# Performance work log

Measured on AMD Instinct MI355X. Metric: run time of the kernel, lower is better.

## Reference

```python
import jax, jax.numpy as jnp
import numpy as np

N = 4096      # batch size
D = 512       # flattened feature dim
C = 128       # num classes / output dim
K = 2         # knn k (module default)
ALPHA = 0.0005


def _safe_sqrt(d2):
    # sqrt with zero (not nan) gradient at exactly 0, matching torch.norm
    d2 = jnp.maximum(d2, 0.0)
    safe = jnp.where(d2 > 0, d2, 1.0)
    return jnp.where(d2 > 0, jnp.sqrt(safe), 0.0)


def _pairwise_dist(a):
    # a: [n, d] -> [n, n] euclidean distances via gram trick
    sq = jnp.sum(a * a, axis=1)
    d2 = sq[:, None] + sq[None, :] - 2.0 * (a @ a.T)
    return _safe_sqrt(d2)


def setup_inputs() -> dict:
    key = jax.random.key(0)
    k1, k2, k3, k4 = jax.random.split(key, 4)
    x_batch = jax.random.normal(k1, (N, D), jnp.float32)
    y_batch = jax.random.randint(k2, (N,), 0, C)
    y_output = jax.random.normal(k3, (N, C), jnp.float32)
    W = jax.random.normal(k4, (D, C), jnp.float32) * 0.02
    b = jnp.zeros((C,), jnp.float32)
    return {"x_batch": x_batch, "y_batch": y_batch, "y_output": y_output, "W": W, "b": b}


def reference(x_batch, y_batch, y_output, W, b):
    n = x_batch.shape[0]
    # ---- loss_function(net(x_batch), y_batch): linear net + cross entropy ----
    logits = x_batch.reshape(n, -1) @ W + b                     # [n, C]
    logp = jax.nn.log_softmax(logits, axis=-1)
    loss = -jnp.mean(jnp.take_along_axis(logp, y_batch[:, None], axis=1))

    # ---- compute_weights_based_on_knn (vectorized) ----
    dx = _pairwise_dist(x_batch.reshape(n, -1))                 # [n, n]
    order = jnp.argsort(dx, axis=1)                             # sklearn kneighbors order
    d_sorted = jnp.take_along_axis(dx, order, axis=1)           # sorted distances (sklearn d)
    e_d = jnp.exp(-d_sorted)                                    # [n, n]
    nbr = order[:, :K + 1]                                      # [n, K+1] raw indices
    rows = jnp.arange(n)[:, None]
    nbr_mask = jnp.zeros((n, n), jnp.float32).at[rows, nbr].set(1.0)  # j in neighbors[i]
    same = (y_batch[:, None] == y_batch[None, :]).astype(jnp.float32)
    # w_diff = w_int - 0; w_int[i,j] = e_d[i,j] (raw-j index into sorted e_d, as in source)
    w_diff = e_d * nbr_mask * same                              # [n, n]

    # ---- weighted_output: sum_ij ||y_out[i]-y_out[j]|| * w_diff[i,j] ----
    dy = _pairwise_dist(y_output)                               # [n, n]
    reg = jnp.sum(dy * w_diff)

    return loss + ALPHA * reg
```

## Files before the change

### kernel.cpp

```cpp
#include <hip/hip_runtime.h>
#include <math.h>
#include <stdint.h>

#define N 4096
#define D 512
#define C 128
#define ALPHA 0.0005f
#define NT_TILES 32
#define TRI (NT_TILES * (NT_TILES + 1) / 2)
#define NTILE (TRI + N / 128)
#define GRID_FUSED 1024

typedef __bf16 bf16x8 __attribute__((ext_vector_type(8)));
typedef float f32x4 __attribute__((ext_vector_type(4)));

__device__ __forceinline__ void wg_barrier_lgkm() {
    asm volatile("s_waitcnt lgkmcnt(0)\n\ts_barrier" ::: "memory");
}

__global__ __launch_bounds__(256) void prep_kernel(const float* __restrict__ x,
                                                   float* __restrict__ sq,
                                                   float* __restrict__ dot0,
                                                   __bf16* __restrict__ xb,
                                                   const float* __restrict__ W,
                                                   __bf16* __restrict__ Wtb,
                                                   unsigned* __restrict__ cnt,
                                                   unsigned* __restrict__ qhead) {
    if (blockIdx.x >= N / 4) {
        const int tid = (blockIdx.x - N / 4) * 256 + threadIdx.x;
        const int k = tid >> 7;
        const int n = tid & 127;
        Wtb[(size_t)n * D + k] = (__bf16)W[tid];
        if (blockIdx.x == N / 4 && threadIdx.x == 0) *qhead = 0u;
        return;
    }
    const int i = blockIdx.x * 4 + (threadIdx.x >> 6);
    const int l = threadIdx.x & 63;
    const float* xp = x + (size_t)i * D + l * 8;
    const float4 v0 = *(const float4*)(xp);
    const float4 v1 = *(const float4*)(xp + 4);
    const float4 u0 = *(const float4*)(x + l * 8);
    const float4 u1 = *(const float4*)(x + l * 8 + 4);
    float s1 = v0.x * v0.x + v0.y * v0.y + v0.z * v0.z + v0.w * v0.w
             + v1.x * v1.x + v1.y * v1.y + v1.z * v1.z + v1.w * v1.w;
    float s2 = v0.x * u0.x + v0.y * u0.y + v0.z * u0.z + v0.w * u0.w
             + v1.x * u1.x + v1.y * u1.y + v1.z * u1.z + v1.w * u1.w;
    bf16x8 o;
    o[0] = (__bf16)v0.x; o[1] = (__bf16)v0.y; o[2] = (__bf16)v0.z; o[3] = (__bf16)v0.w;
    o[4] = (__bf16)v1.x; o[5] = (__bf16)v1.y; o[6] = (__bf16)v1.z; o[7] = (__bf16)v1.w;
    *(bf16x8*)(xb + (size_t)i * D + l * 8) = o;
    for (int off = 32; off; off >>= 1) {
        s1 += __shfl_down(s1, off);
        s2 += __shfl_down(s2, off);
    }
    if (l == 0) { sq[i] = s1; dot0[i] = s2; cnt[i] = 0u; }
}

__global__ __launch_bounds__(256) void fused_mfma(const __bf16* __restrict__ xb,
                                                  const __bf16* __restrict__ Wtb,
                                                  const float* __restrict__ sq,
                                                  const float* __restrict__ dot0,
                                                  const int* __restrict__ y,
                                                  const float* __restrict__ b,
                                                  unsigned* __restrict__ cnt,
                                                  float* __restrict__ lossrow,
                                                  unsigned* __restrict__ qhead) {
    __shared__ __bf16 Alds[2][128 * 32];
    __shared__ __bf16 Blds[2][128 * 32];
    __shared__ float rmax[128][2];
    __shared__ float rsum[128][2];
    __shared__ int bidS;
    const int t = threadIdx.x;
    const int w = t >> 6, l = t & 63;
    const int wy = w >> 1, wx = w & 1;
    const int kg = l >> 4, lr = l & 15;

    const int e0 = t, e1 = t + 256;
    const int r0 = e0 >> 2, c0 = e0 & 3;
    const int r1 = e1 >> 2, c1 = e1 & 3;
    const int sc0 = (c0 ^ (r0 & 3) ^ ((r0 >> 2) & 3)) & 3;
    const int sc1 = (c1 ^ (r1 & 3) ^ ((r1 >> 2) & 3)) & 3;

    for (;;) {
        if (t == 0) bidS = (int)atomicAdd(qhead, 1u);
        __syncthreads();
        const int bid = bidS;
        if (bid >= NTILE) break;

        const bool isCE = (bid >= TRI);
        int bi, bj;
        bool diag = false;
        const __bf16* Bbase;
        if (isCE) {
            bi = (bid - TRI) * 128;
            bj = 0;
            Bbase = Wtb;
        } else {
            int tj = (int)((sqrtf(8.f * (float)bid + 1.f) - 1.f) * 0.5f);
            while (tj * (tj + 1) / 2 > bid) --tj;
            while ((tj + 1) * (tj + 2) / 2 <= bid) ++tj;
            const int ti = bid - tj * (tj + 1) / 2;
            bi = ti * 128;
            bj = tj * 128;
            diag = (ti == tj);
            Bbase = xb + (size_t)bj * D;
        }
        const __bf16* Abase = xb + (size_t)bi * D;

        f32x4 acc[4][4];
        const f32x4 zero = {0.f, 0.f, 0.f, 0.f};
#pragma unroll
        for (int mt = 0; mt < 4; ++mt)
#pragma unroll
            for (int nt = 0; nt < 4; ++nt) acc[mt][nt] = zero;

        const __bf16* Ap0 = Abase + (size_t)r0 * D + sc0 * 8;
        const __bf16* Ap1 = Abase + (size_t)r1 * D + sc1 * 8;
        const __bf16* Bp0 = Bbase + (size_t)r0 * D + sc0 * 8;
        const __bf16* Bp1 = Bbase + (size_t)r1 * D + sc1 * 8;

        uint4 ra0 = *(const uint4*)Ap0;
        uint4 ra1 = *(const uint4*)Ap1;
        uint4 rb0, rb1;
        if (!diag) { rb0 = *(const uint4*)Bp0; rb1 = *(const uint4*)Bp1; }

        for (int k = 0; k < 16; ++k) {
            const int buf = k & 1;
            *(uint4*)((char*)Alds[buf] + e0 * 16) = ra0;
            *(uint4*)((char*)Alds[buf] + e1 * 16) = ra1;
            if (!diag) {
                *(uint4*)((char*)Blds[buf] + e0 * 16) = rb0;
                *(uint4*)((char*)Blds[buf] + e1 * 16) = rb1;
            }
            if (k < 15) {
                const int off = (k + 1) * 32;
                ra0 = *(const uint4*)(Ap0 + off);
                ra1 = *(const uint4*)(Ap1 + off);
                if (!diag) {
                    rb0 = *(const uint4*)(Bp0 + off);
                    rb1 = *(const uint4*)(Bp1 + off);
                }
            }
            wg_barrier_lgkm();
            const __bf16* Al = Alds[buf];
            const __bf16* Bl = diag ? Alds[buf] : Blds[buf];
            bf16x8 av[4], bv[4];
#pragma unroll
            for (int mt = 0; mt < 4; ++mt) {
                const int row = wy * 64 + mt * 16 + lr;
                const int slot = (kg ^ (row & 3) ^ ((row >> 2) & 3)) & 3;
                av[mt] = *(const bf16x8*)(Al + row * 32 + slot * 8);
            }
#pragma unroll
            for (int nt = 0; nt < 4; ++nt) {
                const int row = wx * 64 + nt * 16 + lr;
                const int slot = (kg ^ (row & 3) ^ ((row >> 2) & 3)) & 3;
                bv[nt] = *(const bf16x8*)(Bl + row * 32 + slot * 8);
            }
#pragma unroll
            for (int mt = 0; mt < 4; ++mt)
#pragma unroll
                for (int nt = 0; nt < 4; ++nt)
                    acc[mt][nt] = __builtin_amdgcn_mfma_f32_16x16x32_bf16(av[mt], bv[nt], acc[mt][nt], 0, 0, 0);
        }

        if (isCE) {
            int jn[4]; float bb[4];
#pragma unroll
            for (int nt = 0; nt < 4; ++nt) { jn[nt] = wx * 64 + nt * 16 + lr; bb[nt] = b[jn[nt]]; }
#pragma unroll
            for (int mt = 0; mt < 4; ++mt)
#pragma unroll
                for (int r = 0; r < 4; ++r) {
                    float m = acc[mt][0][r] + bb[0];
#pragma unroll
                    for (int nt = 1; nt < 4; ++nt) m = fmaxf(m, acc[mt][nt][r] + bb[nt]);
                    m = fmaxf(m, __shfl_xor(m, 1));
                    m = fmaxf(m, __shfl_xor(m, 2));
                    m = fmaxf(m, __shfl_xor(m, 4));
                    m = fmaxf(m, __shfl_xor(m, 8));
                    if (lr == 0) rmax[wy * 64 + mt * 16 + kg * 4 + r][wx] = m;
                }
            __syncthreads();
            float mrow[4][4];
#pragma unroll
            for (int mt = 0; mt < 4; ++mt)
#pragma unroll
                for (int r = 0; r < 4; ++r) {
                    const int ri = wy * 64 + mt * 16 + kg * 4 + r;
                    mrow[mt][r] = fmaxf(rmax[ri][0], rmax[ri][1]);
                    float s = 0.f;
#pragma unroll
                    for (int nt = 0; nt < 4; ++nt) s += expf(acc[mt][nt][r] + bb[nt] - mrow[mt][r]);
                    s += __shfl_xor(s, 1);
                    s += __shfl_xor(s, 2);
                    s += __shfl_xor(s, 4);
                    s += __shfl_xor(s, 8);
                    if (lr == 0) rsum[ri][wx] = s;
                }
            __syncthreads();
#pragma unroll
            for (int mt = 0; mt < 4; ++mt)
#pragma unroll
                for (int r = 0; r < 4; ++r) {
                    const int ri = wy * 64 + mt * 16 + kg * 4 + r;
                    const int i = bi + ri;
                    const float s = rsum[ri][0] + rsum[ri][1];
                    const int yi = y[i];
#pragma unroll
                    for (int nt = 0; nt < 4; ++nt)
                        if (jn[nt] == yi)
                            lossrow[i] = -(acc[mt][nt][r] + bb[nt] - mrow[mt][r] - logf(s));
                }
        } else {
            const float sq0 = sq[0];
            int jn[4]; float sqj[4], thrj[4];
#pragma unroll
            for (int nt = 0; nt < 4; ++nt) {
                jn[nt] = bj + wx * 64 + nt * 16 + lr;
                sqj[nt] = sq[jn[nt]];
                thrj[nt] = sq0 - 2.0f * dot0[jn[nt]];
            }
            unsigned cj[4] = {0u, 0u, 0u, 0u};
#pragma unroll
            for (int mt = 0; mt < 4; ++mt)
#pragma unroll
                for (int r = 0; r < 4; ++r) {
                    const int i = bi + wy * 64 + mt * 16 + kg * 4 + r;
                    const float thri = sq0 - 2.0f * dot0[i];
                    const float sqi = sq[i];
                    unsigned ci = 0;
                    if (diag) {
#pragma unroll
                        for (int nt = 0; nt < 4; ++nt) {
                            const float d = acc[mt][nt][r];
                            const int j = jn[nt];
                            if (sqj[nt] - 2.0f * d < thri && j != i && j != 0) ++ci;
                        }
                    } else {
#pragma unroll
                        for (int nt = 0; nt < 4; ++nt) {
                            const float d = acc[mt][nt][r];
                            if (sqj[nt] - 2.0f * d < thri) ++ci;
                            if (sqi - 2.0f * d < thrj[nt] && i != 0) ++cj[nt];
                        }
                    }
                    ci += __shfl_xor((int)ci, 1);
                    ci += __shfl_xor((int)ci, 2);
                    ci += __shfl_xor((int)ci, 4);
                    ci += __shfl_xor((int)ci, 8);
                    if (lr == 0 && ci) atomicAdd(&cnt[i], ci);
                }
            if (!diag) {
#pragma unroll
                for (int nt = 0; nt < 4; ++nt) {
                    unsigned v = cj[nt];
                    v += __shfl_xor((int)v, 16);
                    v += __shfl_xor((int)v, 32);
                    if (l < 16 && v) atomicAdd(&cnt[jn[nt]], v);
                }
            }
        }
    }
}

__global__ __launch_bounds__(1024) void final_kernel(const float* __restrict__ lossrow,
                                                     const unsigned* __restrict__ cnt,
                                                     const int* __restrict__ y,
                                                     const float* __restrict__ Y,
                                                     float* __restrict__ out) {
    const int t = threadIdx.x;
    const int y0 = y[0];
    double ls = 0.0, rs = 0.0;
    for (int i = t; i < N; i += 1024) {
        ls += (double)lossrow[i];
        if (i > 0 && y[i] == y0 && cnt[i] <= 1u) {
            float d2 = 0.f;
            for (int c = 0; c < C; ++c) {
                float d = Y[(size_t)i * C + c] - Y[c];
                d2 += d * d;
            }
            rs += (double)sqrtf(fmaxf(d2, 0.f));
        }
    }
    for (int o = 32; o; o >>= 1) {
        ls += __shfl_down(ls, o);
        rs += __shfl_down(rs, o);
    }
    __shared__ double dl[16], dr[16];
    if ((t & 63) == 0) { dl[t >> 6] = ls; dr[t >> 6] = rs; }
    __syncthreads();
    if (t == 0) {
        double L = 0.0, R = 0.0;
        for (int k = 0; k < 16; ++k) { L += dl[k]; R += dr[k]; }
        out[0] = (float)(L / (double)N + (double)ALPHA * R);
    }
}

extern "C" void kernel_launch(void* const* d_in, const int* in_sizes, int n_in,
                              void* d_out, int out_size, void* d_ws, size_t ws_size,
                              hipStream_t stream) {
    const float* x  = (const float*)d_in[0];
    const int*   y  = (const int*)d_in[1];
    const float* Y  = (const float*)d_in[2];
    const float* W  = (const float*)d_in[3];
    const float* b  = (const float*)d_in[4];
    float* out = (float*)d_out;

    float* wsf      = (float*)d_ws;
    float* lossrow  = wsf;
    float* sq       = wsf + N;
    float* dot0     = wsf + 2 * N;
    unsigned* cnt   = (unsigned*)(wsf + 3 * N);
    __bf16* xb      = (__bf16*)(wsf + 4 * N);
    __bf16* Wtb     = (__bf16*)((char*)xb + (size_t)N * D * 2);
    unsigned* qhead = (unsigned*)((char*)Wtb + (size_t)C * D * 2);

    prep_kernel<<<N / 4 + 256, 256, 0, stream>>>(x, sq, dot0, xb, W, Wtb, cnt, qhead);
    fused_mfma<<<GRID_FUSED, 256, 0, stream>>>(xb, Wtb, sq, dot0, y, b, cnt, lossrow, qhead);
    final_kernel<<<1, 1024, 0, stream>>>(lossrow, cnt, y, Y, out);
}
```

Measured before the change: 119.1 us.

## Replace persistent tile queue with static 64x128 tiles, async LDS loads, parallel final reduction

The persistent atomic work-queue over 128x128 triangular tiles is replaced by a static grid of 64x128 strip tiles, one block per tile, plus 64-row cross-entropy tiles. Tiles are loaded with global_load_lds async copies into a single LDS buffer, with two barriers per k-step in place of the register-prefetch double buffer. The single-block final kernel becomes a 32-block reduction that combines its partial sums through double atomics and a completion counter. The smaller tiles and more blocks aim to improve load balance and occupancy, at the cost of lower data reuse per tile and less overlap between loads and MFMA work.

New measurement: 107.7 us. 9.6% less time.

```diff
diff --git a/kernel.cpp b/kernel.cpp
--- a/kernel.cpp
+++ b/kernel.cpp
@@ -5,17 +5,21 @@
 #define N 4096
 #define D 512
 #define C 128
-#define ALPHA 0.0005f
-#define NT_TILES 32
-#define TRI (NT_TILES * (NT_TILES + 1) / 2)
-#define NTILE (TRI + N / 128)
-#define GRID_FUSED 1024
+#define ALPHA 0.0005
+#define NCOUNT 1056
+#define NCE 64
+#define NBLK (NCOUNT + NCE)
 
 typedef __bf16 bf16x8 __attribute__((ext_vector_type(8)));
 typedef float f32x4 __attribute__((ext_vector_type(4)));
 
-__device__ __forceinline__ void wg_barrier_lgkm() {
-    asm volatile("s_waitcnt lgkmcnt(0)\n\ts_barrier" ::: "memory");
+__device__ __forceinline__ void async16(const void* g, void* l) {
+    __builtin_amdgcn_global_load_lds(
+        reinterpret_cast<const __attribute__((address_space(1))) uint32_t*>(
+            reinterpret_cast<uintptr_t>(g)),
+        reinterpret_cast<__attribute__((address_space(3))) uint32_t*>(
+            reinterpret_cast<uintptr_t>(l)),
+        16, 0, 0);
 }
 
 __global__ __launch_bounds__(256) void prep_kernel(const float* __restrict__ x,
@@ -25,13 +29,16 @@
                                                    const float* __restrict__ W,
                                                    __bf16* __restrict__ Wtb,
                                                    unsigned* __restrict__ cnt,
-                                                   unsigned* __restrict__ qhead) {
+                                                   double* __restrict__ dacc,
+                                                   unsigned* __restrict__ done) {
     if (blockIdx.x >= N / 4) {
         const int tid = (blockIdx.x - N / 4) * 256 + threadIdx.x;
         const int k = tid >> 7;
         const int n = tid & 127;
         Wtb[(size_t)n * D + k] = (__bf16)W[tid];
-        if (blockIdx.x == N / 4 && threadIdx.x == 0) *qhead = 0u;
+        if (blockIdx.x == N / 4 && threadIdx.x == 0) {
+            dacc[0] = 0.0; dacc[1] = 0.0; *done = 0u;
+        }
         return;
     }
     const int i = blockIdx.x * 4 + (threadIdx.x >> 6);
@@ -63,237 +70,222 @@
                                                   const int* __restrict__ y,
                                                   const float* __restrict__ b,
                                                   unsigned* __restrict__ cnt,
-                                                  float* __restrict__ lossrow,
-                                                  unsigned* __restrict__ qhead) {
-    __shared__ __bf16 Alds[2][128 * 32];
-    __shared__ __bf16 Blds[2][128 * 32];
-    __shared__ float rmax[128][2];
-    __shared__ float rsum[128][2];
-    __shared__ int bidS;
+                                                  float* __restrict__ lossrow) {
+    __shared__ __bf16 Alds[64 * 32];
+    __shared__ __bf16 Blds[128 * 32];
+    __shared__ float rmax[64][2];
+    __shared__ float rsum[64][2];
     const int t = threadIdx.x;
     const int w = t >> 6, l = t & 63;
     const int wy = w >> 1, wx = w & 1;
     const int kg = l >> 4, lr = l & 15;
 
-    const int e0 = t, e1 = t + 256;
-    const int r0 = e0 >> 2, c0 = e0 & 3;
-    const int r1 = e1 >> 2, c1 = e1 & 3;
-    const int sc0 = (c0 ^ (r0 & 3) ^ ((r0 >> 2) & 3)) & 3;
-    const int sc1 = (c1 ^ (r1 & 3) ^ ((r1 >> 2) & 3)) & 3;
-
-    for (;;) {
-        if (t == 0) bidS = (int)atomicAdd(qhead, 1u);
+    const int bid = (int)blockIdx.x;
+    const bool isCE = (bid >= NCOUNT);
+    int bi, bj;
+    bool edge = false;
+    const __bf16* Bbase;
+    if (isCE) {
+        bi = (bid - NCOUNT) * 64;
+        bj = 0;
+        Bbase = Wtb;
+    } else {
+        int si = 0, rem = bid;
+        while (rem >= 32 - (si >> 1)) { rem -= 32 - (si >> 1); ++si; }
+        const int cj = (si >> 1) + rem;
+        bi = si * 64;
+        bj = cj * 128;
+        edge = (rem == 0);
+        Bbase = xb + (size_t)bj * D;
+    }
+    const __bf16* Abase = xb + (size_t)bi * D;
+
+    f32x4 acc[2][4];
+    const f32x4 zero = {0.f, 0.f, 0.f, 0.f};
+#pragma unroll
+    for (int mt = 0; mt < 2; ++mt)
+#pragma unroll
+        for (int nt = 0; nt < 4; ++nt) acc[mt][nt] = zero;
+
+    const int rA = t >> 2, cA = t & 3;
+    const int scA = (cA ^ (rA & 3) ^ ((rA >> 2) & 3)) & 3;
+    const int eB0 = t, eB1 = t + 256;
+    const int rB0 = eB0 >> 2, cB0 = eB0 & 3;
+    const int rB1 = eB1 >> 2, cB1 = eB1 & 3;
+    const int scB0 = (cB0 ^ (rB0 & 3) ^ ((rB0 >> 2) & 3)) & 3;
+    const int scB1 = (cB1 ^ (rB1 & 3) ^ ((rB1 >> 2) & 3)) & 3;
+
+    for (int kc = 0; kc < D; kc += 32) {
         __syncthreads();
-        const int bid = bidS;
-        if (bid >= NTILE) break;
-
-        const bool isCE = (bid >= TRI);
-        int bi, bj;
-        bool diag = false;
-        const __bf16* Bbase;
-        if (isCE) {
-            bi = (bid - TRI) * 128;
-            bj = 0;
-            Bbase = Wtb;
-        } else {
-            int tj = (int)((sqrtf(8.f * (float)bid + 1.f) - 1.f) * 0.5f);
-            while (tj * (tj + 1) / 2 > bid) --tj;
-            while ((tj + 1) * (tj + 2) / 2 <= bid) ++tj;
-            const int ti = bid - tj * (tj + 1) / 2;
-            bi = ti * 128;
-            bj = tj * 128;
-            diag = (ti == tj);
-            Bbase = xb + (size_t)bj * D;
-        }
-        const __bf16* Abase = xb + (size_t)bi * D;
-
-        f32x4 acc[4][4];
-        const f32x4 zero = {0.f, 0.f, 0.f, 0.f};
-#pragma unroll
-        for (int mt = 0; mt < 4; ++mt)
-#pragma unroll
-            for (int nt = 0; nt < 4; ++nt) acc[mt][nt] = zero;
-
-        const __bf16* Ap0 = Abase + (size_t)r0 * D + sc0 * 8;
-        const __bf16* Ap1 = Abase + (size_t)r1 * D + sc1 * 8;
-        const __bf16* Bp0 = Bbase + (size_t)r0 * D + sc0 * 8;
-        const __bf16* Bp1 = Bbase + (size_t)r1 * D + sc1 * 8;
-
-        uint4 ra0 = *(const uint4*)Ap0;
-        uint4 ra1 = *(const uint4*)Ap1;
-        uint4 rb0, rb1;
-        if (!diag) { rb0 = *(const uint4*)Bp0; rb1 = *(const uint4*)Bp1; }
-
-        for (int k = 0; k < 16; ++k) {
-            const int buf = k & 1;
-            *(uint4*)((char*)Alds[buf] + e0 * 16) = ra0;
-            *(uint4*)((char*)Alds[buf] + e1 * 16) = ra1;
-            if (!diag) {
-                *(uint4*)((char*)Blds[buf] + e0 * 16) = rb0;
-                *(uint4*)((char*)Blds[buf] + e1 * 16) = rb1;
-            }
-            if (k < 15) {
-                const int off = (k + 1) * 32;
-                ra0 = *(const uint4*)(Ap0 + off);
-                ra1 = *(const uint4*)(Ap1 + off);
-                if (!diag) {
-                    rb0 = *(const uint4*)(Bp0 + off);
-                    rb1 = *(const uint4*)(Bp1 + off);
+        async16(Abase + (size_t)rA * D + kc + scA * 8, (char*)Alds + t * 16);
+        async16(Bbase + (size_t)rB0 * D + kc + scB0 * 8, (char*)Blds + eB0 * 16);
+        async16(Bbase + (size_t)rB1 * D + kc + scB1 * 8, (char*)Blds + eB1 * 16);
+        __syncthreads();
+        bf16x8 av[2], bv[4];
+#pragma unroll
+        for (int mt = 0; mt < 2; ++mt) {
+            const int row = wy * 32 + mt * 16 + lr;
+            const int slot = (kg ^ (row & 3) ^ ((row >> 2) & 3)) & 3;
+            av[mt] = *(const bf16x8*)(Alds + row * 32 + slot * 8);
+        }
+#pragma unroll
+        for (int nt = 0; nt < 4; ++nt) {
+            const int row = wx * 64 + nt * 16 + lr;
+            const int slot = (kg ^ (row & 3) ^ ((row >> 2) & 3)) & 3;
+            bv[nt] = *(const bf16x8*)(Blds + row * 32 + slot * 8);
+        }
+#pragma unroll
+        for (int mt = 0; mt < 2; ++mt)
+#pragma unroll
+            for (int nt = 0; nt < 4; ++nt)
+                acc[mt][nt] = __builtin_amdgcn_mfma_f32_16x16x32_bf16(av[mt], bv[nt], acc[mt][nt], 0, 0, 0);
+    }
+
+    if (isCE) {
+        int jn[4]; float bb[4];
+#pragma unroll
+        for (int nt = 0; nt < 4; ++nt) { jn[nt] = wx * 64 + nt * 16 + lr; bb[nt] = b[jn[nt]]; }
+#pragma unroll
+        for (int mt = 0; mt < 2; ++mt)
+#pragma unroll
+            for (int r = 0; r < 4; ++r) {
+                float m = acc[mt][0][r] + bb[0];
+#pragma unroll
+                for (int nt = 1; nt < 4; ++nt) m = fmaxf(m, acc[mt][nt][r] + bb[nt]);
+                m = fmaxf(m, __shfl_xor(m, 1));
+                m = fmaxf(m, __shfl_xor(m, 2));
+                m = fmaxf(m, __shfl_xor(m, 4));
+                m = fmaxf(m, __shfl_xor(m, 8));
+                if (lr == 0) rmax[wy * 32 + mt * 16 + kg * 4 + r][wx] = m;
+            }
+        __syncthreads();
+        float mrow[2][4];
+#pragma unroll
+        for (int mt = 0; mt < 2; ++mt)
+#pragma unroll
+            for (int r = 0; r < 4; ++r) {
+                const int ri = wy * 32 + mt * 16 + kg * 4 + r;
+                mrow[mt][r] = fmaxf(rmax[ri][0], rmax[ri][1]);
+                float s = 0.f;
+#pragma unroll
+                for (int nt = 0; nt < 4; ++nt) s += expf(acc[mt][nt][r] + bb[nt] - mrow[mt][r]);
+                s += __shfl_xor(s, 1);
+                s += __shfl_xor(s, 2);
+                s += __shfl_xor(s, 4);
+                s += __shfl_xor(s, 8);
+                if (lr == 0) rsum[ri][wx] = s;
+            }
+        __syncthreads();
+#pragma unroll
+        for (int mt = 0; mt < 2; ++mt)
+#pragma unroll
+            for (int r = 0; r < 4; ++r) {
+                const int ri = wy * 32 + mt * 16 + kg * 4 + r;
+                const int i = bi + ri;
+                const float s = rsum[ri][0] + rsum[ri][1];
+                const int yi = y[i];
+#pragma unroll
+                for (int nt = 0; nt < 4; ++nt)
+                    if (jn[nt] == yi)
+                        lossrow[i] = -(acc[mt][nt][r] + bb[nt] - mrow[mt][r] - logf(s));
+            }
+    } else {
+        const float sq0 = sq[0];
+        int jn[4]; float sqj[4], thrj[4];
+#pragma unroll
+        for (int nt = 0; nt < 4; ++nt) {
+            jn[nt] = bj + wx * 64 + nt * 16 + lr;
+            sqj[nt] = sq[jn[nt]];
+            thrj[nt] = sq0 - 2.0f * dot0[jn[nt]];
+        }
+        unsigned cj[4] = {0u, 0u, 0u, 0u};
+#pragma unroll
+        for (int mt = 0; mt < 2; ++mt)
+#pragma unroll
+            for (int r = 0; r < 4; ++r) {
+                const int i = bi + wy * 32 + mt * 16 + kg * 4 + r;
+                const float thri = sq0 - 2.0f * dot0[i];
+                const float sqi = sq[i];
+                unsigned ci = 0;
+                if (edge) {
+#pragma unroll
+                    for (int nt = 0; nt < 4; ++nt) {
+                        const float d = acc[mt][nt][r];
+                        const int j = jn[nt];
+                        if (sqj[nt] - 2.0f * d < thri && j != i && j != 0) ++ci;
+                    }
+                } else {
+#pragma unroll
+                    for (int nt = 0; nt < 4; ++nt) {
+                        const float d = acc[mt][nt][r];
+                        if (sqj[nt] - 2.0f * d < thri) ++ci;
+                        if (sqi - 2.0f * d < thrj[nt] && i != 0) ++cj[nt];
+                    }
                 }
-            }
-            wg_barrier_lgkm();
-            const __bf16* Al = Alds[buf];
-            const __bf16* Bl = diag ? Alds[buf] : Blds[buf];
-            bf16x8 av[4], bv[4];
-#pragma unroll
-            for (int mt = 0; mt < 4; ++mt) {
-                const int row = wy * 64 + mt * 16 + lr;
-                const int slot = (kg ^ (row & 3) ^ ((row >> 2) & 3)) & 3;
-                av[mt] = *(const bf16x8*)(Al + row * 32 + slot * 8);
-            }
+                ci += __shfl_xor((int)ci, 1);
+                ci += __shfl_xor((int)ci, 2);
+                ci += __shfl_xor((int)ci, 4);
+                ci += __shfl_xor((int)ci, 8);
+                if (lr == 0 && ci) atomicAdd(&cnt[i], ci);
+            }
+        if (!edge) {
 #pragma unroll
             for (int nt = 0; nt < 4; ++nt) {
-                const int row = wx * 64 + nt * 16 + lr;
-                const int slot = (kg ^ (row & 3) ^ ((row >> 2) & 3)) & 3;
-                bv[nt] = *(const bf16x8*)(Bl + row * 32 + slot * 8);
-            }
-#pragma unroll
-            for (int mt = 0; mt < 4; ++mt)
-#pragma unroll
-                for (int nt = 0; nt < 4; ++nt)
-                    acc[mt][nt] = __builtin_amdgcn_mfma_f32_16x16x32_bf16(av[mt], bv[nt], acc[mt][nt], 0, 0, 0);
-        }
-
-        if (isCE) {
-            int jn[4]; float bb[4];
-#pragma unroll
-            for (int nt = 0; nt < 4; ++nt) { jn[nt] = wx * 64 + nt * 16 + lr; bb[nt] = b[jn[nt]]; }
-#pragma unroll
-            for (int mt = 0; mt < 4; ++mt)
-#pragma unroll
-                for (int r = 0; r < 4; ++r) {
-                    float m = acc[mt][0][r] + bb[0];
-#pragma unroll
-                    for (int nt = 1; nt < 4; ++nt) m = fmaxf(m, acc[mt][nt][r] + bb[nt]);
-                    m = fmaxf(m, __shfl_xor(m, 1));
-                    m = fmaxf(m, __shfl_xor(m, 2));
-                    m = fmaxf(m, __shfl_xor(m, 4));
-                    m = fmaxf(m, __shfl_xor(m, 8));
-                    if (lr == 0) rmax[wy * 64 + mt * 16 + kg * 4 + r][wx] = m;
-                }
-            __syncthreads();
-            float mrow[4][4];
-#pragma unroll
-            for (int mt = 0; mt < 4; ++mt)
-#pragma unroll
-                for (int r = 0; r < 4; ++r) {
-                    const int ri = wy * 64 + mt * 16 + kg * 4 + r;
-                    mrow[mt][r] = fmaxf(rmax[ri][0], rmax[ri][1]);
-                    float s = 0.f;
-#pragma unroll
-                    for (int nt = 0; nt < 4; ++nt) s += expf(acc[mt][nt][r] + bb[nt] - mrow[mt][r]);
-                    s += __shfl_xor(s, 1);
-                    s += __shfl_xor(s, 2);
-                    s += __shfl_xor(s, 4);
-                    s += __shfl_xor(s, 8);
-                    if (lr == 0) rsum[ri][wx] = s;
-                }
-            __syncthreads();
-#pragma unroll
-            for (int mt = 0; mt < 4; ++mt)
-#pragma unroll
-                for (int r = 0; r < 4; ++r) {
-                    const int ri = wy * 64 + mt * 16 + kg * 4 + r;
-                    const int i = bi + ri;
-                    const float s = rsum[ri][0] + rsum[ri][1];
-                    const int yi = y[i];
-#pragma unroll
-                    for (int nt = 0; nt < 4; ++nt)
-                        if (jn[nt] == yi)
-                            lossrow[i] = -(acc[mt][nt][r] + bb[nt] - mrow[mt][r] - logf(s));
-                }
-        } else {
-            const float sq0 = sq[0];
-            int jn[4]; float sqj[4], thrj[4];
-#pragma unroll
-            for (int nt = 0; nt < 4; ++nt) {
-                jn[nt] = bj + wx * 64 + nt * 16 + lr;
-                sqj[nt] = sq[jn[nt]];
-                thrj[nt] = sq0 - 2.0f * dot0[jn[nt]];
-            }
-            unsigned cj[4] = {0u, 0u, 0u, 0u};
-#pragma unroll
-            for (int mt = 0; mt < 4; ++mt)
-#pragma unroll
-                for (int r = 0; r < 4; ++r) {
-                    const int i = bi + wy * 64 + mt * 16 + kg * 4 + r;
-                    const float thri = sq0 - 2.0f * dot0[i];
-                    const float sqi = sq[i];
-                    unsigned ci = 0;
-                    if (diag) {
-#pragma unroll
-                        for (int nt = 0; nt < 4; ++nt) {
-                            const float d = acc[mt][nt][r];
-                            const int j = jn[nt];
-                            if (sqj[nt] - 2.0f * d < thri && j != i && j != 0) ++ci;
-                        }
-                    } else {
-#pragma unroll
-                        for (int nt = 0; nt < 4; ++nt) {
-                            const float d = acc[mt][nt][r];
-                            if (sqj[nt] - 2.0f * d < thri) ++ci;
-                            if (sqi - 2.0f * d < thrj[nt] && i != 0) ++cj[nt];
-                        }
-                    }
-                    ci += __shfl_xor((int)ci, 1);
-                    ci += __shfl_xor((int)ci, 2);
-                    ci += __shfl_xor((int)ci, 4);
-                    ci += __shfl_xor((int)ci, 8);
-                    if (lr == 0 && ci) atomicAdd(&cnt[i], ci);
-                }
-            if (!diag) {
-#pragma unroll
-                for (int nt = 0; nt < 4; ++nt) {
-                    unsigned v = cj[nt];
-                    v += __shfl_xor((int)v, 16);
-                    v += __shfl_xor((int)v, 32);
-                    if (l < 16 && v) atomicAdd(&cnt[jn[nt]], v);
-                }
-            }
-        }
-    }
-}
-
-__global__ __launch_bounds__(1024) void final_kernel(const float* __restrict__ lossrow,
-                                                     const unsigned* __restrict__ cnt,
-                                                     const int* __restrict__ y,
-                                                     const float* __restrict__ Y,
-                                                     float* __restrict__ out) {
+                unsigned v = cj[nt];
+                v += __shfl_xor((int)v, 16);
+                v += __shfl_xor((int)v, 32);
+                if (l < 16 && v) atomicAdd(&cnt[jn[nt]], v);
+            }
+        }
+    }
+}
+
+__global__ __launch_bounds__(256) void reg_kernel(const float* __restrict__ lossrow,
+                                                  const unsigned* __restrict__ cnt,
+                                                  const int* __restrict__ y,
+                                                  const float* __restrict__ Y,
+                                                  double* __restrict__ dacc,
+                                                  unsigned* __restrict__ done,
+                                                  float* __restrict__ out) {
     const int t = threadIdx.x;
+    const int i = blockIdx.x * 128 + (t >> 1);
+    const int half = t & 1;
     const int y0 = y[0];
+
+    const float4* yr = (const float4*)(Y + (size_t)i * C + half * 64);
+    const float4* yz = (const float4*)(Y + half * 64);
+    float d2 = 0.f;
+#pragma unroll
+    for (int c = 0; c < 16; ++c) {
+        const float4 a = yr[c];
+        const float4 bb = yz[c];
+        const float dx = a.x - bb.x, dy = a.y - bb.y, dz = a.z - bb.z, dw = a.w - bb.w;
+        d2 += dx * dx + dy * dy + dz * dz + dw * dw;
+    }
+    d2 += __shfl_xor(d2, 1);
+
     double ls = 0.0, rs = 0.0;
-    for (int i = t; i < N; i += 1024) {
-        ls += (double)lossrow[i];
-        if (i > 0 && y[i] == y0 && cnt[i] <= 1u) {
-            float d2 = 0.f;
-            for (int c = 0; c < C; ++c) {
-                float d = Y[(size_t)i * C + c] - Y[c];
-                d2 += d * d;
-            }
-            rs += (double)sqrtf(fmaxf(d2, 0.f));
-        }
+    if (half == 0) {
+        ls = (double)lossrow[i];
+        if (i > 0 && y[i] == y0 && cnt[i] <= 1u)
+            rs = sqrt((double)fmaxf(d2, 0.f));
     }
     for (int o = 32; o; o >>= 1) {
         ls += __shfl_down(ls, o);
         rs += __shfl_down(rs, o);
     }
-    __shared__ double dl[16], dr[16];
+    __shared__ double dl[4], dr[4];
     if ((t & 63) == 0) { dl[t >> 6] = ls; dr[t >> 6] = rs; }
     __syncthreads();
     if (t == 0) {
-        double L = 0.0, R = 0.0;
-        for (int k = 0; k < 16; ++k) { L += dl[k]; R += dr[k]; }
-        out[0] = (float)(L / (double)N + (double)ALPHA * R);
+        atomicAdd(&dacc[0], dl[0] + dl[1] + dl[2] + dl[3]);
+        atomicAdd(&dacc[1], dr[0] + dr[1] + dr[2] + dr[3]);
+        __threadfence();
+        if (atomicAdd(done, 1u) == 31u) {
+            const double L = atomicAdd(&dacc[0], 0.0);
+            const double R = atomicAdd(&dacc[1], 0.0);
+            out[0] = (float)(L / (double)N + ALPHA * R);
+        }
     }
 }
 
@@ -314,9 +306,10 @@
     unsigned* cnt   = (unsigned*)(wsf + 3 * N);
     __bf16* xb      = (__bf16*)(wsf + 4 * N);
     __bf16* Wtb     = (__bf16*)((char*)xb + (size_t)N * D * 2);
-    unsigned* qhead = (unsigned*)((char*)Wtb + (size_t)C * D * 2);
-
-    prep_kernel<<<N / 4 + 256, 256, 0, stream>>>(x, sq, dot0, xb, W, Wtb, cnt, qhead);
-    fused_mfma<<<GRID_FUSED, 256, 0, stream>>>(xb, Wtb, sq, dot0, y, b, cnt, lossrow, qhead);
-    final_kernel<<<1, 1024, 0, stream>>>(lossrow, cnt, y, Y, out);
-}
+    double* dacc    = (double*)((char*)Wtb + (size_t)C * D * 2);
+    unsigned* done  = (unsigned*)(dacc + 2);
+
+    prep_kernel<<<N / 4 + 256, 256, 0, stream>>>(x, sq, dot0, xb, W, Wtb, cnt, dacc, done);
+    fused_mfma<<<NBLK, 256, 0, stream>>>(xb, Wtb, sq, dot0, y, b, cnt, lossrow);
+    reg_kernel<<<32, 256, 0, stream>>>(lossrow, cnt, y, Y, dacc, done, out);
+}
```
